# Kernel tuning notes

Hardware: AMD Instinct MI355X
Metric: run time of the kernel (lower is better)

## Reference

```python
import jax, jax.numpy as jnp
import numpy as np

TAU_PLUS = 0.02
TAU_MINUS = 0.02
TAU_X = 0.101
A_TRIPLET = 0.0065
HOMEOSTATIC_RATE = 0.1
DT = 0.001
SPIKE_P = 0.05  # spike probability used to binarize inputs


def setup_inputs() -> dict:
    key = jax.random.key(0)
    k1, k2, k3 = jax.random.split(key, 3)
    B, P, Q, T = 16, 2048, 2048, 256
    pre_spikes = (jax.random.uniform(k1, (B, P, T)) < SPIKE_P).astype(jnp.float32)
    post_spikes = (jax.random.uniform(k2, (B, Q, T)) < SPIKE_P).astype(jnp.float32)
    weights = jax.random.normal(k3, (P, Q), dtype=jnp.float32) * 0.1
    meta_A_plus = jnp.float32(0.01)
    meta_A_minus = jnp.float32(0.012)
    return {"pre_spikes": pre_spikes, "post_spikes": post_spikes,
            "weights": weights, "meta_A_plus": meta_A_plus,
            "meta_A_minus": meta_A_minus}


def _traces(spikes_tbn, decay):
    """Trace value used at step t: x_t = decay * (x_{t-1} + s_{t-1}), x_0 = 0."""
    def step(carry, s):
        x = decay * carry          # decayed trace, used for this step's update
        return x + s, x            # spike added AFTER the update, per original
    init = jnp.zeros(spikes_tbn.shape[1:], spikes_tbn.dtype)
    _, xs = jax.lax.scan(step, init, spikes_tbn)
    return xs  # [T, B, N]


def reference(pre_spikes, post_spikes, weights, meta_A_plus, meta_A_minus):
    B, P, T = pre_spikes.shape
    exp_plus = jnp.exp(jnp.float32(-DT / TAU_PLUS))
    exp_minus = jnp.exp(jnp.float32(-DT / TAU_MINUS))
    exp_x = jnp.exp(jnp.float32(-DT / TAU_X))

    pre_t = jnp.transpose(pre_spikes, (2, 0, 1))    # [T, B, P]
    post_t = jnp.transpose(post_spikes, (2, 0, 1))  # [T, B, Q]

    x_pre = _traces(pre_t, exp_plus)     # [T, B, P]
    x_post = _traces(post_t, exp_minus)  # [T, B, Q]
    x_trip = _traces(post_t, exp_x)      # [T, B, Q]

    # Per-step outer products summed over time == one big contraction over (t, b).
    ltp = jnp.einsum('tbp,tbq->pq', x_pre, post_t) * meta_A_plus
    triplet = jnp.einsum('tbp,tbq->pq', x_pre, post_t * x_trip) * A_TRIPLET
    ltd = jnp.einsum('tbp,tbq->pq', pre_t, x_post) * meta_A_minus
    weight_updates = ltp + triplet - ltd

    # Homeostatic scaling (fresh module: activity history holds only this sample)
    current_activity = (pre_spikes.sum() + post_spikes.sum()) / (B * T)
    scaling_factor = jnp.sqrt(HOMEOSTATIC_RATE / (current_activity + 1e-6))

    updated_weights = weights + weight_updates * scaling_factor
    return jnp.clip(updated_weights, -2.0, 2.0)
```

## Files before the change

kernel.cpp:

```cpp
#include <hip/hip_runtime.h>


constexpr int TB = 16;
constexpr int NP = 2048;
constexpr int NQ = 2048;
constexpr int TT = 256;
constexpr int KH = TB * TT;
constexpr int KT = 2 * KH;

typedef unsigned short ushort_t;
typedef __attribute__((ext_vector_type(8))) __bf16 bf16x8;
typedef __attribute__((ext_vector_type(4))) float f32x4;

__device__ __forceinline__ unsigned bf1(float f) {
    unsigned u = __builtin_bit_cast(unsigned, f);
    return (u + 0x7FFFu + ((u >> 16) & 1u)) >> 16;
}
__device__ __forceinline__ unsigned pack2(float lo, float hi) {
    return bf1(lo) | (bf1(hi) << 16);
}
__device__ __forceinline__ unsigned spk2(float a, float b) {
    return ((a != 0.f) ? 0x3F80u : 0u) | ((b != 0.f) ? 0x3F800000u : 0u);
}

constexpr float DF1 = 0.95122942450071400910f;
constexpr float DF2 = DF1 * DF1;
constexpr float DF4 = DF2 * DF2;
constexpr float DF8 = DF4 * DF4;
constexpr float DF16 = DF8 * DF8;
constexpr float DF32 = DF16 * DF16;
constexpr float DF64 = DF32 * DF32;

constexpr float DX1 = 0.99014786386058731819f;
constexpr float DX2 = DX1 * DX1;
constexpr float DX4 = DX2 * DX2;
constexpr float DX8 = DX4 * DX4;
constexpr float DX16 = DX8 * DX8;
constexpr float DX32 = DX16 * DX16;
constexpr float DX64 = DX32 * DX32;

template <int K>
__device__ __forceinline__ float seg_step(float b, float pw, int sl) {
    float t = __shfl_up(b, K, 64);
    return (sl >= K) ? fmaf(pw, t, b) : b;
}
__device__ __forceinline__ float scan16(float c, float p1, float p2, float p4,
                                        float p8, int sl) {
    c = seg_step<1>(c, p1, sl);
    c = seg_step<2>(c, p2, sl);
    c = seg_step<4>(c, p4, sl);
    c = seg_step<8>(c, p8, sl);
    return c;
}
__device__ __forceinline__ float fold4(float4 u, float d) {
    float C = d * u.x;
    C = d * (C + u.y); C = d * (C + u.z); C = d * (C + u.w);
    return C;
}
__device__ __forceinline__ float4 expand4(float x, float4 u, float d) {
    float4 t;
    t.x = x; x = d * (x + u.x);
    t.y = x; x = d * (x + u.y);
    t.z = x; x = d * (x + u.z);
    t.w = x;
    return t;
}

__global__ __launch_bounds__(256) void stage_traces(
    const float* __restrict__ pre, const float* __restrict__ post,
    const float* __restrict__ mApP, const float* __restrict__ mAmP,
    ushort_t* __restrict__ Ab, ushort_t* __restrict__ Bb,
    float* __restrict__ partials)
{
    const int tid  = threadIdx.x;
    const int lane = tid & 63;
    const int wv   = tid >> 6;
    const int sl   = lane & 15;
    const int rowg = blockIdx.x * 16 + wv * 4 + (lane >> 4);
    const bool isPre = rowg < TB * NP;
    const int m = isPre ? rowg : rowg - TB * NP;
    const int b = m >> 11;
    const int r = m & 2047;

    const float4* srcRow = (const float4*)((isPre ? pre : post) + (size_t)m * TT);
    const float4 u0 = srcRow[sl];
    const float4 u1 = srcRow[16 + sl];
    const float4 u2 = srcRow[32 + sl];
    const float4 u3 = srcRow[48 + sl];

    float cnt = ((u0.x + u0.y) + (u0.z + u0.w)) + ((u1.x + u1.y) + (u1.z + u1.w))
              + ((u2.x + u2.y) + (u2.z + u2.w)) + ((u3.x + u3.y) + (u3.z + u3.w));

    const int hi = lane | 15;

    float bf0 = scan16(fold4(u0, DF1), DF4, DF8, DF16, DF32, sl);
    float bf1_ = scan16(fold4(u1, DF1), DF4, DF8, DF16, DF32, sl);
    float bf2 = scan16(fold4(u2, DF1), DF4, DF8, DF16, DF32, sl);
    float bf3 = scan16(fold4(u3, DF1), DF4, DF8, DF16, DF32, sl);
    const float Tf0 = __shfl(bf0, hi, 64);
    const float Tf1 = __shfl(bf1_, hi, 64);
    const float Tf2 = __shfl(bf2, hi, 64);
    const float Xf1 = Tf0;
    const float Xf2 = fmaf(DF64, Xf1, Tf1);
    const float Xf3 = fmaf(DF64, Xf2, Tf2);
    float ef0 = __shfl_up(bf0, 1, 64);
    float ef1 = __shfl_up(bf1_, 1, 64);
    float ef2 = __shfl_up(bf2, 1, 64);
    float ef3 = __shfl_up(bf3, 1, 64);
    if (sl == 0) { ef0 = 0.f; ef1 = 0.f; ef2 = 0.f; ef3 = 0.f; }
    float pf = 1.f;
    if (sl & 1) pf *= DF4;
    if (sl & 2) pf *= DF8;
    if (sl & 4) pf *= DF16;
    if (sl & 8) pf *= DF32;
    const float4 t0 = expand4(ef0,                 u0, DF1);
    const float4 t1 = expand4(fmaf(pf, Xf1, ef1),  u1, DF1);
    const float4 t2 = expand4(fmaf(pf, Xf2, ef2),  u2, DF1);
    const float4 t3 = expand4(fmaf(pf, Xf3, ef3),  u3, DF1);

    ushort_t* oA = (isPre ? Ab : Bb) + (size_t)r * KT + b * TT + 4 * sl;

    if (isPre) {
        *(uint2*)(oA)            = uint2{pack2(t0.x, t0.y), pack2(t0.z, t0.w)};
        *(uint2*)(oA + 64)       = uint2{pack2(t1.x, t1.y), pack2(t1.z, t1.w)};
        *(uint2*)(oA + 128)      = uint2{pack2(t2.x, t2.y), pack2(t2.z, t2.w)};
        *(uint2*)(oA + 192)      = uint2{pack2(t3.x, t3.y), pack2(t3.z, t3.w)};
        *(uint2*)(oA + KH)       = uint2{spk2(u0.x, u0.y), spk2(u0.z, u0.w)};
        *(uint2*)(oA + KH + 64)  = uint2{spk2(u1.x, u1.y), spk2(u1.z, u1.w)};
        *(uint2*)(oA + KH + 128) = uint2{spk2(u2.x, u2.y), spk2(u2.z, u2.w)};
        *(uint2*)(oA + KH + 192) = uint2{spk2(u3.x, u3.y), spk2(u3.z, u3.w)};
    } else {
        float bx0 = scan16(fold4(u0, DX1), DX4, DX8, DX16, DX32, sl);
        float bx1 = scan16(fold4(u1, DX1), DX4, DX8, DX16, DX32, sl);
        float bx2 = scan16(fold4(u2, DX1), DX4, DX8, DX16, DX32, sl);
        float bx3 = scan16(fold4(u3, DX1), DX4, DX8, DX16, DX32, sl);
        const float Tx0 = __shfl(bx0, hi, 64);
        const float Tx1 = __shfl(bx1, hi, 64);
        const float Tx2 = __shfl(bx2, hi, 64);
        const float Xx1 = Tx0;
        const float Xx2 = fmaf(DX64, Xx1, Tx1);
        const float Xx3 = fmaf(DX64, Xx2, Tx2);
        float ex0 = __shfl_up(bx0, 1, 64);
        float ex1 = __shfl_up(bx1, 1, 64);
        float ex2 = __shfl_up(bx2, 1, 64);
        float ex3 = __shfl_up(bx3, 1, 64);
        if (sl == 0) { ex0 = 0.f; ex1 = 0.f; ex2 = 0.f; ex3 = 0.f; }
        float px = 1.f;
        if (sl & 1) px *= DX4;
        if (sl & 2) px *= DX8;
        if (sl & 4) px *= DX16;
        if (sl & 8) px *= DX32;
        const float4 w0 = expand4(ex0,                u0, DX1);
        const float4 w1 = expand4(fmaf(px, Xx1, ex1), u1, DX1);
        const float4 w2 = expand4(fmaf(px, Xx2, ex2), u2, DX1);
        const float4 w3 = expand4(fmaf(px, Xx3, ex3), u3, DX1);

        const float Ap = *mApP;
        const float Am = *mAmP;
        auto av2 = [&](float sa, float ta, float sb, float tb) -> unsigned {
            unsigned lo = (sa != 0.f) ? bf1(fmaf(0.0065f, ta, Ap)) : 0u;
            unsigned hi2 = (sb != 0.f) ? bf1(fmaf(0.0065f, tb, Ap)) : 0u;
            return lo | (hi2 << 16);
        };
        *(uint2*)(oA)       = uint2{av2(u0.x, w0.x, u0.y, w0.y), av2(u0.z, w0.z, u0.w, w0.w)};
        *(uint2*)(oA + 64)  = uint2{av2(u1.x, w1.x, u1.y, w1.y), av2(u1.z, w1.z, u1.w, w1.w)};
        *(uint2*)(oA + 128) = uint2{av2(u2.x, w2.x, u2.y, w2.y), av2(u2.z, w2.z, u2.w, w2.w)};
        *(uint2*)(oA + 192) = uint2{av2(u3.x, w3.x, u3.y, w3.y), av2(u3.z, w3.z, u3.w, w3.w)};
        *(uint2*)(oA + KH)       = uint2{pack2(-Am * t0.x, -Am * t0.y), pack2(-Am * t0.z, -Am * t0.w)};
        *(uint2*)(oA + KH + 64)  = uint2{pack2(-Am * t1.x, -Am * t1.y), pack2(-Am * t1.z, -Am * t1.w)};
        *(uint2*)(oA + KH + 128) = uint2{pack2(-Am * t2.x, -Am * t2.y), pack2(-Am * t2.z, -Am * t2.w)};
        *(uint2*)(oA + KH + 192) = uint2{pack2(-Am * t3.x, -Am * t3.y), pack2(-Am * t3.z, -Am * t3.w)};
    }

    #pragma unroll
    for (int off = 32; off > 0; off >>= 1)
        cnt += __shfl_down(cnt, off, 64);
    __shared__ float wsum[4];
    if (lane == 0) wsum[wv] = cnt;
    __syncthreads();
    if (tid == 0)
        partials[blockIdx.x] = (wsum[0] + wsum[1]) + (wsum[2] + wsum[3]);
}

__device__ __forceinline__ void async16(const ushort_t* g, ushort_t* l) {
    __builtin_amdgcn_global_load_lds(
        (const __attribute__((address_space(1))) unsigned int*)g,
        (__attribute__((address_space(3))) unsigned int*)l,
        16, 0, 0);
}

__global__ __launch_bounds__(256, 2) void gemm_split(
    const ushort_t* __restrict__ Ab, const ushort_t* __restrict__ Bb,
    const float* __restrict__ sp, float* __restrict__ scaleBuf,
    float* __restrict__ P0, float* __restrict__ P1)
{
    __shared__ ushort_t As[2][128 * 64];
    __shared__ ushort_t Bs[2][128 * 64];
    __shared__ float red[4];

    const int tid  = threadIdx.x;
    const int lane = tid & 63;
    const int wv   = tid >> 6;
    const int wr   = wv >> 1;
    const int wc   = wv & 1;
    const int quad = lane >> 4;
    const int m16  = lane & 15;

    if (blockIdx.x == 0) {
        float v = 0.f;
        #pragma unroll
        for (int i = 0; i < 16; ++i) v += sp[tid + i * 256];
        #pragma unroll
        for (int off = 32; off > 0; off >>= 1)
            v += __shfl_down(v, off, 64);
        if (lane == 0) red[wv] = v;
        __syncthreads();
        if (tid == 0) {
            float s = (red[0] + red[1]) + (red[2] + red[3]);
            scaleBuf[0] = sqrtf(0.1f / (s * (1.0f / 4096.0f) + 1e-6f));
        }
    }

    const int id  = blockIdx.x;
    const int xcd = id & 7;
    const int j5  = id >> 3;
    const int z   = j5 & 1;
    const int t   = j5 >> 1;
    const int pt  = ((xcd >> 1) << 2) + (t >> 3);
    const int qt  = ((xcd & 1) << 3) + (t & 7);

    const int p0 = pt * 128;
    const int q0 = qt * 128;
    const int kbase = z * (KT / 2);
    const int ldsbase = wv * 512;

    const ushort_t* gaP[4];
    const ushort_t* gbP[4];
    #pragma unroll
    for (int rr = 0; rr < 4; ++rr) {
        const int c   = rr * 256 + tid;
        const int row = c >> 3;
        const int kk8 = (c & 7) ^ (row & 7);
        gaP[rr] = Ab + (size_t)(p0 + row) * KT + kbase + kk8 * 8;
        gbP[rr] = Bb + (size_t)(q0 + row) * KT + kbase + kk8 * 8;
    }

    f32x4 acc[4][4] = {};

    auto stageF = [&](int buf) {
        #pragma unroll
        for (int rr = 0; rr < 4; ++rr) {
            async16(gaP[rr], &As[buf][rr * 2048 + ldsbase]);
            async16(gbP[rr], &Bs[buf][rr * 2048 + ldsbase]);
            gaP[rr] += 64;
            gbP[rr] += 64;
        }
    };
    auto computeF = [&](int buf) {
        #pragma unroll
        for (int ks = 0; ks < 2; ++ks) {
            bf16x8 af[4], bfr[4];
            #pragma unroll
            for (int i = 0; i < 4; ++i) {
                const int row  = wr * 64 + i * 16 + m16;
                const int slot = (ks * 4 + quad) ^ (row & 7);
                af[i] = *(const bf16x8*)&As[buf][row * 64 + slot * 8];
            }
            #pragma unroll
            for (int jj = 0; jj < 4; ++jj) {
                const int row  = wc * 64 + jj * 16 + m16;
                const int slot = (ks * 4 + quad) ^ (row & 7);
                bfr[jj] = *(const bf16x8*)&Bs[buf][row * 64 + slot * 8];
            }
            #pragma unroll
            for (int i = 0; i < 4; ++i)
                #pragma unroll
                for (int jj = 0; jj < 4; ++jj)
                    acc[i][jj] = __builtin_amdgcn_mfma_f32_16x16x32_bf16(
                        af[i], bfr[jj], acc[i][jj], 0, 0, 0);
        }
    };

    constexpr int NIT = (KT / 2) / 64;
    stageF(0);
    for (int kt2 = 0; kt2 < NIT / 2; ++kt2) {
        __syncthreads();
        stageF(1);
        computeF(0);
        __syncthreads();
        if (kt2 + 1 < NIT / 2)
            stageF(0);
        computeF(1);
    }

    float* P = z ? P1 : P0;
    #pragma unroll
    for (int i = 0; i < 4; ++i) {
        const int prow = p0 + wr * 64 + i * 16 + quad * 4;
        #pragma unroll
        for (int jj = 0; jj < 4; ++jj) {
            const int qcol = q0 + wc * 64 + jj * 16 + m16;
            #pragma unroll
            for (int r2 = 0; r2 < 4; ++r2)
                P[(size_t)(prow + r2) * NQ + qcol] = acc[i][jj][r2];
        }
    }
}

__global__ __launch_bounds__(256) void merge_out(
    const float* __restrict__ W, const float* __restrict__ P1,
    const float* __restrict__ scaleBuf, float* __restrict__ Out)
{
    const float scale = scaleBuf[0];
    const size_t i4 = (size_t)blockIdx.x * 256 + threadIdx.x;
    float4 w = ((const float4*)W)[i4];
    float4 a = ((const float4*)Out)[i4];
    float4 c = ((const float4*)P1)[i4];
    float4 o;
    o.x = fminf(fmaxf(fmaf(scale, a.x + c.x, w.x), -2.f), 2.f);
    o.y = fminf(fmaxf(fmaf(scale, a.y + c.y, w.y), -2.f), 2.f);
    o.z = fminf(fmaxf(fmaf(scale, a.z + c.z, w.z), -2.f), 2.f);
    o.w = fminf(fmaxf(fmaf(scale, a.w + c.w, w.w), -2.f), 2.f);
    ((float4*)Out)[i4] = o;
}

extern "C" void kernel_launch(void* const* d_in, const int* in_sizes, int n_in,
                              void* d_out, int out_size, void* d_ws, size_t ws_size,
                              hipStream_t stream) {
    const float* pre  = (const float*)d_in[0];
    const float* post = (const float*)d_in[1];
    const float* W    = (const float*)d_in[2];
    const float* mAp  = (const float*)d_in[3];
    const float* mAm  = (const float*)d_in[4];
    float* out = (float*)d_out;

    char* ws = (char*)d_ws;
    float* partials = (float*)ws;
    float* scaleBuf = (float*)(ws + 16384);
    ushort_t* Ab = (ushort_t*)(ws + 32768);
    ushort_t* Bb = (ushort_t*)(ws + 32768 + (size_t)NP * KT * 2);
    float* P1    = (float*)(ws + 32768 + 2 * (size_t)NP * KT * 2);

    stage_traces<<<dim3((TB * NP + TB * NQ) / 16), dim3(256), 0, stream>>>(
        pre, post, mAp, mAm, Ab, Bb, partials);

    gemm_split<<<dim3(512), dim3(256), 0, stream>>>(
        Ab, Bb, partials, scaleBuf, out, P1);

    merge_out<<<dim3(NP * NQ / 1024), dim3(256), 0, stream>>>(
        W, P1, scaleBuf, out);
}
```

Measured before the change: 200.2 us.

## Add 256x256-tile 8-wave GEMM with 4-way split-K and ping-pong schedule

Adds a new 512-thread GEMM that computes a 256x256 output tile per block, splits K four ways, and maps blocks to XCDs so neighbouring tiles share L2. Its main loop interleaves LDS reads, async global-to-LDS staging and MFMA quarter-blocks, separated by explicit barriers and waitcnts and raised with setprio. The larger tile raises operand reuse and cuts global traffic. The cost is an extra partial buffer pair to write and merge in a four-input merge kernel. The new path runs only when the workspace is large enough, otherwise the old 128x128 split-2 path is used.

```diff
diff --git a/kernel.cpp b/kernel.cpp
--- a/kernel.cpp
+++ b/kernel.cpp
@@ -189,13 +189,192 @@
         16, 0, 0);
 }
 
+#define FENCE() asm volatile("" ::: "memory")
+#define BAR()   do { FENCE(); __builtin_amdgcn_s_barrier(); FENCE(); } while (0)
+#define LGKM0() asm volatile("s_waitcnt lgkmcnt(0)" ::: "memory")
+#define VMC2()  asm volatile("s_waitcnt vmcnt(2)" ::: "memory")
+#define VMC0()  asm volatile("s_waitcnt vmcnt(0)" ::: "memory")
+
+#define STAGE(GP, LP, KI, H) do {                                           \
+    const ushort_t* _g = (GP) + (size_t)(H) * 128 * KT + (size_t)(KI) * 64; \
+    ushort_t* _l = (LP) + (H) * 8192;                                       \
+    async16(_g + ofG,  _l + ld0);                                           \
+    async16(_g + ofG2, _l + ld1);                                           \
+} while (0)
+
+#define RD_A(BUF, QM) do {                                                  \
+    _Pragma("unroll")                                                       \
+    for (int mi = 0; mi < 4; ++mi) {                                        \
+        const ushort_t* _r = &As[BUF][aBase + (QM) * 4096 + mi * 1024];     \
+        af[mi][0] = *(const bf16x8*)(_r + sK0);                             \
+        af[mi][1] = *(const bf16x8*)(_r + sK1);                             \
+    }                                                                       \
+} while (0)
+
+#define RD_B(BUF, QN, BV) do {                                              \
+    _Pragma("unroll")                                                       \
+    for (int ni = 0; ni < 2; ++ni) {                                        \
+        const ushort_t* _r = &Bs[BUF][bBase + (QN) * 2048 + ni * 1024];     \
+        BV[ni][0] = *(const bf16x8*)(_r + sK0);                             \
+        BV[ni][1] = *(const bf16x8*)(_r + sK1);                             \
+    }                                                                       \
+} while (0)
+
+#define MFMAQ(QM, QN, BV) do {                                              \
+    __builtin_amdgcn_s_setprio(1);                                          \
+    _Pragma("unroll")                                                       \
+    for (int ks = 0; ks < 2; ++ks)                                          \
+        _Pragma("unroll")                                                   \
+        for (int mi = 0; mi < 4; ++mi)                                      \
+            _Pragma("unroll")                                               \
+            for (int ni = 0; ni < 2; ++ni)                                  \
+                acc[(QM)*4+mi][(QN)*2+ni] =                                 \
+                    __builtin_amdgcn_mfma_f32_16x16x32_bf16(                \
+                        af[mi][ks], BV[ni][ks],                             \
+                        acc[(QM)*4+mi][(QN)*2+ni], 0, 0, 0);                \
+    __builtin_amdgcn_s_setprio(0);                                          \
+} while (0)
+
+__global__ __launch_bounds__(512) void gemm8(
+    const ushort_t* __restrict__ Ab, const ushort_t* __restrict__ Bb,
+    const float* __restrict__ sp, float* __restrict__ scaleBuf,
+    float* __restrict__ P0, float* __restrict__ P1,
+    float* __restrict__ P2, float* __restrict__ P3)
+{
+    __shared__ ushort_t As[2][256 * 64];
+    __shared__ ushort_t Bs[2][256 * 64];
+    __shared__ float red[8];
+
+    const int tid  = threadIdx.x;
+    const int lane = tid & 63;
+    const int wv   = tid >> 6;
+    const int wr   = wv >> 2;
+    const int wc   = wv & 3;
+    const int quad = lane >> 4;
+    const int m16  = lane & 15;
+
+    if (blockIdx.x == 0) {
+        float v = 0.f;
+        #pragma unroll
+        for (int i = 0; i < 8; ++i) v += sp[tid + i * 512];
+        #pragma unroll
+        for (int off = 32; off > 0; off >>= 1)
+            v += __shfl_down(v, off, 64);
+        if (lane == 0) red[wv] = v;
+        __syncthreads();
+        if (tid == 0) {
+            float s = ((red[0] + red[1]) + (red[2] + red[3]))
+                    + ((red[4] + red[5]) + (red[6] + red[7]));
+            scaleBuf[0] = sqrtf(0.1f / (s * (1.0f / 4096.0f) + 1e-6f));
+        }
+    }
+
+    const int id  = blockIdx.x;
+    const int xcd = id & 7;
+    const int j   = id >> 3;
+    const int z   = j & 3;
+    const int t   = j >> 2;
+    const int pt  = ((xcd >> 1) << 1) | (t >> 2);
+    const int qt  = ((xcd & 1) << 2) | (t & 3);
+    const int p0  = pt * 256;
+    const int q0  = qt * 256;
+    const int kbase = z * (KT / 4);
+
+    const ushort_t* Agp = Ab + (size_t)p0 * KT + kbase;
+    const ushort_t* Bgp = Bb + (size_t)q0 * KT + kbase;
+    const int rIn  = tid >> 3;
+    const int rIn2 = rIn + 64;
+    const size_t ofG  = (size_t)rIn  * KT + (size_t)((((tid & 7) ^ (rIn  & 7))) * 8);
+    const size_t ofG2 = (size_t)rIn2 * KT + (size_t)((((tid & 7) ^ (rIn2 & 7))) * 8);
+    const int ld0 = tid * 8;
+    const int ld1 = 4096 + tid * 8;
+
+    const int x8  = (m16 & 7) * 8;
+    const int sK0 = (quad * 8) ^ x8;
+    const int sK1 = ((quad + 4) * 8) ^ x8;
+    const int aBase = (wr * 128 + m16) * 64;
+    const int bBase = (wc * 64 + m16) * 64;
+
+    f32x4 acc[8][4] = {};
+    bf16x8 af[4][2], bv0[2][2], bv1[2][2];
+
+    STAGE(Agp, As[0], 0, 0);
+    STAGE(Agp, As[0], 0, 1);
+    STAGE(Bgp, Bs[0], 0, 0);
+    STAGE(Bgp, Bs[0], 0, 1);
+    STAGE(Agp, As[1], 1, 0);
+    VMC2();
+    BAR();
+
+    #pragma unroll 1
+    for (int it = 0; it < 16; ++it) {
+        const int k2 = 2 * it;
+        RD_A(0, 0);
+        RD_B(0, 0, bv0);
+        STAGE(Agp, As[1], k2 + 1, 1);
+        STAGE(Bgp, Bs[1], k2 + 1, 0);
+        BAR(); LGKM0();
+        MFMAQ(0, 0, bv0);
+        BAR();
+        RD_B(0, 1, bv1);
+        STAGE(Bgp, Bs[1], k2 + 1, 1);
+        BAR(); LGKM0();
+        MFMAQ(0, 1, bv1);
+        BAR();
+        RD_A(0, 1);
+        BAR(); LGKM0();
+        MFMAQ(1, 1, bv1);
+        BAR();
+        RD_B(0, 0, bv0);
+        if (it < 15) STAGE(Agp, As[0], k2 + 2, 0);
+        BAR(); LGKM0();
+        MFMAQ(1, 0, bv0);
+        if (it < 15) { VMC2(); } else { VMC0(); }
+        BAR();
+        RD_A(1, 0);
+        RD_B(1, 0, bv0);
+        if (it < 15) { STAGE(Agp, As[0], k2 + 2, 1); STAGE(Bgp, Bs[0], k2 + 2, 0); }
+        BAR(); LGKM0();
+        MFMAQ(0, 0, bv0);
+        BAR();
+        RD_B(1, 1, bv1);
+        if (it < 15) STAGE(Bgp, Bs[0], k2 + 2, 1);
+        BAR(); LGKM0();
+        MFMAQ(0, 1, bv1);
+        BAR();
+        RD_A(1, 1);
+        BAR(); LGKM0();
+        MFMAQ(1, 1, bv1);
+        BAR();
+        RD_B(1, 0, bv0);
+        if (it < 15) STAGE(Agp, As[1], k2 + 3, 0);
+        BAR(); LGKM0();
+        MFMAQ(1, 0, bv0);
+        if (it < 15) { VMC2(); }
+        BAR();
+    }
+
+    float* P = (z == 0) ? P0 : ((z == 1) ? P1 : ((z == 2) ? P2 : P3));
+    #pragma unroll
+    for (int m = 0; m < 8; ++m) {
+        const int prow = p0 + wr * 128 + m * 16 + quad * 4;
+        #pragma unroll
+        for (int n = 0; n < 4; ++n) {
+            const int qcol = q0 + wc * 64 + n * 16 + m16;
+            #pragma unroll
+            for (int r = 0; r < 4; ++r)
+                P[(size_t)(prow + r) * NQ + qcol] = acc[m][n][r];
+        }
+    }
+}
+
 __global__ __launch_bounds__(256, 2) void gemm_split(
     const ushort_t* __restrict__ Ab, const ushort_t* __restrict__ Bb,
     const float* __restrict__ sp, float* __restrict__ scaleBuf,
     float* __restrict__ P0, float* __restrict__ P1)
 {
-    __shared__ ushort_t As[2][128 * 64];
-    __shared__ ushort_t Bs[2][128 * 64];
+    __shared__ ushort_t Ls[2][128 * 64];
+    __shared__ ushort_t Rs[2][128 * 64];
     __shared__ float red[4];
 
     const int tid  = threadIdx.x;
@@ -250,8 +429,8 @@
     auto stageF = [&](int buf) {
         #pragma unroll
         for (int rr = 0; rr < 4; ++rr) {
-            async16(gaP[rr], &As[buf][rr * 2048 + ldsbase]);
-            async16(gbP[rr], &Bs[buf][rr * 2048 + ldsbase]);
+            async16(gaP[rr], &Ls[buf][rr * 2048 + ldsbase]);
+            async16(gbP[rr], &Rs[buf][rr * 2048 + ldsbase]);
             gaP[rr] += 64;
             gbP[rr] += 64;
         }
@@ -259,25 +438,25 @@
     auto computeF = [&](int buf) {
         #pragma unroll
         for (int ks = 0; ks < 2; ++ks) {
-            bf16x8 af[4], bfr[4];
+            bf16x8 afl[4], bfr[4];
             #pragma unroll
             for (int i = 0; i < 4; ++i) {
                 const int row  = wr * 64 + i * 16 + m16;
                 const int slot = (ks * 4 + quad) ^ (row & 7);
-                af[i] = *(const bf16x8*)&As[buf][row * 64 + slot * 8];
+                afl[i] = *(const bf16x8*)&Ls[buf][row * 64 + slot * 8];
             }
             #pragma unroll
             for (int jj = 0; jj < 4; ++jj) {
                 const int row  = wc * 64 + jj * 16 + m16;
                 const int slot = (ks * 4 + quad) ^ (row & 7);
-                bfr[jj] = *(const bf16x8*)&Bs[buf][row * 64 + slot * 8];
+                bfr[jj] = *(const bf16x8*)&Rs[buf][row * 64 + slot * 8];
             }
             #pragma unroll
             for (int i = 0; i < 4; ++i)
                 #pragma unroll
                 for (int jj = 0; jj < 4; ++jj)
                     acc[i][jj] = __builtin_amdgcn_mfma_f32_16x16x32_bf16(
-                        af[i], bfr[jj], acc[i][jj], 0, 0, 0);
+                        afl[i], bfr[jj], acc[i][jj], 0, 0, 0);
         }
     };
 
@@ -307,7 +486,27 @@
     }
 }
 
-__global__ __launch_bounds__(256) void merge_out(
+__global__ __launch_bounds__(256) void merge_out4(
+    const float* __restrict__ W, const float* __restrict__ P1,
+    const float* __restrict__ P2, const float* __restrict__ P3,
+    const float* __restrict__ scaleBuf, float* __restrict__ Out)
+{
+    const float scale = scaleBuf[0];
+    const size_t i4 = (size_t)blockIdx.x * 256 + threadIdx.x;
+    float4 w = ((const float4*)W)[i4];
+    float4 a = ((const float4*)Out)[i4];
+    float4 b = ((const float4*)P1)[i4];
+    float4 c = ((const float4*)P2)[i4];
+    float4 d = ((const float4*)P3)[i4];
+    float4 o;
+    o.x = fminf(fmaxf(fmaf(scale, (a.x + b.x) + (c.x + d.x), w.x), -2.f), 2.f);
+    o.y = fminf(fmaxf(fmaf(scale, (a.y + b.y) + (c.y + d.y), w.y), -2.f), 2.f);
+    o.z = fminf(fmaxf(fmaf(scale, (a.z + b.z) + (c.z + d.z), w.z), -2.f), 2.f);
+    o.w = fminf(fmaxf(fmaf(scale, (a.w + b.w) + (c.w + d.w), w.w), -2.f), 2.f);
+    ((float4*)Out)[i4] = o;
+}
+
+__global__ __launch_bounds__(256) void merge_out2(
     const float* __restrict__ W, const float* __restrict__ P1,
     const float* __restrict__ scaleBuf, float* __restrict__ Out)
 {
@@ -334,19 +533,30 @@
     const float* mAm  = (const float*)d_in[4];
     float* out = (float*)d_out;
 
+    const size_t AB = (size_t)NP * KT * 2;
+    const size_t PB = (size_t)NP * NQ * 4;
+
     char* ws = (char*)d_ws;
     float* partials = (float*)ws;
     float* scaleBuf = (float*)(ws + 16384);
     ushort_t* Ab = (ushort_t*)(ws + 32768);
-    ushort_t* Bb = (ushort_t*)(ws + 32768 + (size_t)NP * KT * 2);
-    float* P1    = (float*)(ws + 32768 + 2 * (size_t)NP * KT * 2);
+    ushort_t* Bb = (ushort_t*)(ws + 32768 + AB);
+    float* P1 = (float*)(ws + 32768 + 2 * AB);
+    float* P2 = (float*)(ws + 32768 + 2 * AB + PB);
+    float* P3 = (float*)(ws + 32768 + 2 * AB + 2 * PB);
 
     stage_traces<<<dim3((TB * NP + TB * NQ) / 16), dim3(256), 0, stream>>>(
         pre, post, mAp, mAm, Ab, Bb, partials);
 
-    gemm_split<<<dim3(512), dim3(256), 0, stream>>>(
-        Ab, Bb, partials, scaleBuf, out, P1);
-
-    merge_out<<<dim3(NP * NQ / 1024), dim3(256), 0, stream>>>(
-        W, P1, scaleBuf, out);
-}
+    if (ws_size >= 32768 + 2 * AB + 3 * PB) {
+        gemm8<<<dim3(256), dim3(512), 0, stream>>>(
+            Ab, Bb, partials, scaleBuf, out, P1, P2, P3);
+        merge_out4<<<dim3(NP * NQ / 1024), dim3(256), 0, stream>>>(
+            W, P1, P2, P3, scaleBuf, out);
+    } else {
+        gemm_split<<<dim3(512), dim3(256), 0, stream>>>(
+            Ab, Bb, partials, scaleBuf, out, P1);
+        merge_out2<<<dim3(NP * NQ / 1024), dim3(256), 0, stream>>>(
+            W, P1, scaleBuf, out);
+    }
+}
```

After: 209.7 us. +4.8%, slower.

## Fuse split-K reduction and epilogue into GEMM via per-tile atomic counter

Applied to the files above, without the earlier changes.

Each split-K tile pair now writes its partial product and bumps a per-tile atomic counter. The second block to finish reads the other partial, computes the homeostatic scale itself, and writes the clipped final output, so the separate merge kernel and one full pass over the output are no longer needed. The counters are zeroed by the staging kernel. This trades an extra partial buffer, threadfence and atomic overhead, and a serial tail in the last-arriving block, for one fewer launch and less global traffic. It falls back to the old path when the workspace is too small.

```diff
diff --git a/kernel.cpp b/kernel.cpp
--- a/kernel.cpp
+++ b/kernel.cpp
@@ -70,9 +70,11 @@
     const float* __restrict__ pre, const float* __restrict__ post,
     const float* __restrict__ mApP, const float* __restrict__ mAmP,
     ushort_t* __restrict__ Ab, ushort_t* __restrict__ Bb,
-    float* __restrict__ partials)
+    float* __restrict__ partials, int* __restrict__ cnt)
 {
     const int tid  = threadIdx.x;
+    if (blockIdx.x == 0) cnt[tid] = 0;
+
     const int lane = tid & 63;
     const int wv   = tid >> 6;
     const int sl   = lane & 15;
@@ -88,8 +90,8 @@
     const float4 u2 = srcRow[32 + sl];
     const float4 u3 = srcRow[48 + sl];
 
-    float cnt = ((u0.x + u0.y) + (u0.z + u0.w)) + ((u1.x + u1.y) + (u1.z + u1.w))
-              + ((u2.x + u2.y) + (u2.z + u2.w)) + ((u3.x + u3.y) + (u3.z + u3.w));
+    float cnt_s = ((u0.x + u0.y) + (u0.z + u0.w)) + ((u1.x + u1.y) + (u1.z + u1.w))
+                + ((u2.x + u2.y) + (u2.z + u2.w)) + ((u3.x + u3.y) + (u3.z + u3.w));
 
     const int hi = lane | 15;
 
@@ -174,9 +176,9 @@
 
     #pragma unroll
     for (int off = 32; off > 0; off >>= 1)
-        cnt += __shfl_down(cnt, off, 64);
+        cnt_s += __shfl_down(cnt_s, off, 64);
     __shared__ float wsum[4];
-    if (lane == 0) wsum[wv] = cnt;
+    if (lane == 0) wsum[wv] = cnt_s;
     __syncthreads();
     if (tid == 0)
         partials[blockIdx.x] = (wsum[0] + wsum[1]) + (wsum[2] + wsum[3]);
@@ -189,14 +191,16 @@
         16, 0, 0);
 }
 
-__global__ __launch_bounds__(256, 2) void gemm_split(
+__global__ __launch_bounds__(256, 2) void gemm_fz(
     const ushort_t* __restrict__ Ab, const ushort_t* __restrict__ Bb,
-    const float* __restrict__ sp, float* __restrict__ scaleBuf,
-    float* __restrict__ P0, float* __restrict__ P1)
+    const float* __restrict__ sp, const float* __restrict__ W,
+    float* __restrict__ P0, float* __restrict__ P1,
+    int* __restrict__ cnt, float* __restrict__ Out)
 {
-    __shared__ ushort_t As[2][128 * 64];
-    __shared__ ushort_t Bs[2][128 * 64];
+    __shared__ ushort_t Ls[2][128 * 64];
+    __shared__ ushort_t Rs[2][128 * 64];
     __shared__ float red[4];
+    __shared__ int tk;
 
     const int tid  = threadIdx.x;
     const int lane = tid & 63;
@@ -206,21 +210,6 @@
     const int quad = lane >> 4;
     const int m16  = lane & 15;
 
-    if (blockIdx.x == 0) {
-        float v = 0.f;
-        #pragma unroll
-        for (int i = 0; i < 16; ++i) v += sp[tid + i * 256];
-        #pragma unroll
-        for (int off = 32; off > 0; off >>= 1)
-            v += __shfl_down(v, off, 64);
-        if (lane == 0) red[wv] = v;
-        __syncthreads();
-        if (tid == 0) {
-            float s = (red[0] + red[1]) + (red[2] + red[3]);
-            scaleBuf[0] = sqrtf(0.1f / (s * (1.0f / 4096.0f) + 1e-6f));
-        }
-    }
-
     const int id  = blockIdx.x;
     const int xcd = id & 7;
     const int j5  = id >> 3;
@@ -250,8 +239,8 @@
     auto stageF = [&](int buf) {
         #pragma unroll
         for (int rr = 0; rr < 4; ++rr) {
-            async16(gaP[rr], &As[buf][rr * 2048 + ldsbase]);
-            async16(gbP[rr], &Bs[buf][rr * 2048 + ldsbase]);
+            async16(gaP[rr], &Ls[buf][rr * 2048 + ldsbase]);
+            async16(gbP[rr], &Rs[buf][rr * 2048 + ldsbase]);
             gaP[rr] += 64;
             gbP[rr] += 64;
         }
@@ -259,25 +248,25 @@
     auto computeF = [&](int buf) {
         #pragma unroll
         for (int ks = 0; ks < 2; ++ks) {
-            bf16x8 af[4], bfr[4];
+            bf16x8 afl[4], bfr[4];
             #pragma unroll
             for (int i = 0; i < 4; ++i) {
                 const int row  = wr * 64 + i * 16 + m16;
                 const int slot = (ks * 4 + quad) ^ (row & 7);
-                af[i] = *(const bf16x8*)&As[buf][row * 64 + slot * 8];
+                afl[i] = *(const bf16x8*)&Ls[buf][row * 64 + slot * 8];
             }
             #pragma unroll
             for (int jj = 0; jj < 4; ++jj) {
                 const int row  = wc * 64 + jj * 16 + m16;
                 const int slot = (ks * 4 + quad) ^ (row & 7);
-                bfr[jj] = *(const bf16x8*)&Bs[buf][row * 64 + slot * 8];
+                bfr[jj] = *(const bf16x8*)&Rs[buf][row * 64 + slot * 8];
             }
             #pragma unroll
             for (int i = 0; i < 4; ++i)
                 #pragma unroll
                 for (int jj = 0; jj < 4; ++jj)
                     acc[i][jj] = __builtin_amdgcn_mfma_f32_16x16x32_bf16(
-                        af[i], bfr[jj], acc[i][jj], 0, 0, 0);
+                        afl[i], bfr[jj], acc[i][jj], 0, 0, 0);
         }
     };
 
@@ -305,9 +294,159 @@
                 P[(size_t)(prow + r2) * NQ + qcol] = acc[i][jj][r2];
         }
     }
-}
-
-__global__ __launch_bounds__(256) void merge_out(
+    __threadfence();
+    if (tid == 0) tk = atomicAdd(&cnt[pt * 16 + qt], 1);
+    __syncthreads();
+    if (tk == 0) return;
+    __threadfence();
+
+    float v = 0.f;
+    #pragma unroll
+    for (int i = 0; i < 16; ++i) v += sp[tid + i * 256];
+    #pragma unroll
+    for (int off = 32; off > 0; off >>= 1)
+        v += __shfl_down(v, off, 64);
+    if (lane == 0) red[wv] = v;
+    __syncthreads();
+    const float s = (red[0] + red[1]) + (red[2] + red[3]);
+    const float scale = sqrtf(0.1f / (s * (1.0f / 4096.0f) + 1e-6f));
+
+    const float* Ps = z ? P0 : P1;
+    #pragma unroll
+    for (int i = 0; i < 4; ++i) {
+        const int prow = p0 + wr * 64 + i * 16 + quad * 4;
+        #pragma unroll
+        for (int jj = 0; jj < 4; ++jj) {
+            const int qcol = q0 + wc * 64 + jj * 16 + m16;
+            #pragma unroll
+            for (int r2 = 0; r2 < 4; ++r2) {
+                const size_t idx = (size_t)(prow + r2) * NQ + qcol;
+                const float sum = acc[i][jj][r2] + Ps[idx];
+                Out[idx] = fminf(fmaxf(fmaf(scale, sum, W[idx]), -2.f), 2.f);
+            }
+        }
+    }
+}
+
+__global__ __launch_bounds__(256, 2) void gemm_split(
+    const ushort_t* __restrict__ Ab, const ushort_t* __restrict__ Bb,
+    const float* __restrict__ sp, float* __restrict__ scaleBuf,
+    float* __restrict__ P0, float* __restrict__ P1)
+{
+    __shared__ ushort_t Ls[2][128 * 64];
+    __shared__ ushort_t Rs[2][128 * 64];
+    __shared__ float red[4];
+
+    const int tid  = threadIdx.x;
+    const int lane = tid & 63;
+    const int wv   = tid >> 6;
+    const int wr   = wv >> 1;
+    const int wc   = wv & 1;
+    const int quad = lane >> 4;
+    const int m16  = lane & 15;
+
+    if (blockIdx.x == 0) {
+        float v = 0.f;
+        #pragma unroll
+        for (int i = 0; i < 16; ++i) v += sp[tid + i * 256];
+        #pragma unroll
+        for (int off = 32; off > 0; off >>= 1)
+            v += __shfl_down(v, off, 64);
+        if (lane == 0) red[wv] = v;
+        __syncthreads();
+        if (tid == 0) {
+            float s = (red[0] + red[1]) + (red[2] + red[3]);
+            scaleBuf[0] = sqrtf(0.1f / (s * (1.0f / 4096.0f) + 1e-6f));
+        }
+    }
+
+    const int id  = blockIdx.x;
+    const int xcd = id & 7;
+    const int j5  = id >> 3;
+    const int z   = j5 & 1;
+    const int t   = j5 >> 1;
+    const int pt  = ((xcd >> 1) << 2) + (t >> 3);
+    const int qt  = ((xcd & 1) << 3) + (t & 7);
+
+    const int p0 = pt * 128;
+    const int q0 = qt * 128;
+    const int kbase = z * (KT / 2);
+    const int ldsbase = wv * 512;
+
+    const ushort_t* gaP[4];
+    const ushort_t* gbP[4];
+    #pragma unroll
+    for (int rr = 0; rr < 4; ++rr) {
+        const int c   = rr * 256 + tid;
+        const int row = c >> 3;
+        const int kk8 = (c & 7) ^ (row & 7);
+        gaP[rr] = Ab + (size_t)(p0 + row) * KT + kbase + kk8 * 8;
+        gbP[rr] = Bb + (size_t)(q0 + row) * KT + kbase + kk8 * 8;
+    }
+
+    f32x4 acc[4][4] = {};
+
+    auto stageF = [&](int buf) {
+        #pragma unroll
+        for (int rr = 0; rr < 4; ++rr) {
+            async16(gaP[rr], &Ls[buf][rr * 2048 + ldsbase]);
+            async16(gbP[rr], &Rs[buf][rr * 2048 + ldsbase]);
+            gaP[rr] += 64;
+            gbP[rr] += 64;
+        }
+    };
+    auto computeF = [&](int buf) {
+        #pragma unroll
+        for (int ks = 0; ks < 2; ++ks) {
+            bf16x8 afl[4], bfr[4];
+            #pragma unroll
+            for (int i = 0; i < 4; ++i) {
+                const int row  = wr * 64 + i * 16 + m16;
+                const int slot = (ks * 4 + quad) ^ (row & 7);
+                afl[i] = *(const bf16x8*)&Ls[buf][row * 64 + slot * 8];
+            }
+            #pragma unroll
+            for (int jj = 0; jj < 4; ++jj) {
+                const int row  = wc * 64 + jj * 16 + m16;
+                const int slot = (ks * 4 + quad) ^ (row & 7);
+                bfr[jj] = *(const bf16x8*)&Rs[buf][row * 64 + slot * 8];
+            }
+            #pragma unroll
+            for (int i = 0; i < 4; ++i)
+                #pragma unroll
+                for (int jj = 0; jj < 4; ++jj)
+                    acc[i][jj] = __builtin_amdgcn_mfma_f32_16x16x32_bf16(
+                        afl[i], bfr[jj], acc[i][jj], 0, 0, 0);
+        }
+    };
+
+    constexpr int NIT = (KT / 2) / 64;
+    stageF(0);
+    for (int kt2 = 0; kt2 < NIT / 2; ++kt2) {
+        __syncthreads();
+        stageF(1);
+        computeF(0);
+        __syncthreads();
+        if (kt2 + 1 < NIT / 2)
+            stageF(0);
+        computeF(1);
+    }
+
+    float* P = z ? P1 : P0;
+    #pragma unroll
+    for (int i = 0; i < 4; ++i) {
+        const int prow = p0 + wr * 64 + i * 16 + quad * 4;
+        #pragma unroll
+        for (int jj = 0; jj < 4; ++jj) {
+            const int qcol = q0 + wc * 64 + jj * 16 + m16;
+            #pragma unroll
+            for (int r2 = 0; r2 < 4; ++r2)
+                P[(size_t)(prow + r2) * NQ + qcol] = acc[i][jj][r2];
+        }
+    }
+}
+
+__global__ __launch_bounds__(256) void merge_out2(
     const float* __restrict__ W, const float* __restrict__ P1,
     const float* __restrict__ scaleBuf, float* __restrict__ Out)
 {
@@ -334,19 +473,28 @@
     const float* mAm  = (const float*)d_in[4];
     float* out = (float*)d_out;
 
+    const size_t AB = (size_t)NP * KT * 2;
+    const size_t PB = (size_t)NP * NQ * 4;
+
     char* ws = (char*)d_ws;
     float* partials = (float*)ws;
     float* scaleBuf = (float*)(ws + 16384);
+    int*   cnt      = (int*)(ws + 20480);
     ushort_t* Ab = (ushort_t*)(ws + 32768);
-    ushort_t* Bb = (ushort_t*)(ws + 32768 + (size_t)NP * KT * 2);
-    float* P1    = (float*)(ws + 32768 + 2 * (size_t)NP * KT * 2);
+    ushort_t* Bb = (ushort_t*)(ws + 32768 + AB);
+    float* Pa = (float*)(ws + 32768 + 2 * AB);
+    float* Pb = (float*)(ws + 32768 + 2 * AB + PB);
 
     stage_traces<<<dim3((TB * NP + TB * NQ) / 16), dim3(256), 0, stream>>>(
-        pre, post, mAp, mAm, Ab, Bb, partials);
-
-    gemm_split<<<dim3(512), dim3(256), 0, stream>>>(
-        Ab, Bb, partials, scaleBuf, out, P1);
-
-    merge_out<<<dim3(NP * NQ / 1024), dim3(256), 0, stream>>>(
-        W, P1, scaleBuf, out);
-}
+        pre, post, mAp, mAm, Ab, Bb, partials, cnt);
+
+    if (ws_size >= 32768 + 2 * AB + 2 * PB) {
+        gemm_fz<<<dim3(512), dim3(256), 0, stream>>>(
+            Ab, Bb, partials, W, Pa, Pb, cnt, out);
+    } else {
+        gemm_split<<<dim3(512), dim3(256), 0, stream>>>(
+            Ab, Bb, partials, scaleBuf, out, Pa);
+        merge_out2<<<dim3(NP * NQ / 1024), dim3(256), 0, stream>>>(
+            W, Pa, scaleBuf, out);
+    }
+}
```

Result: slower. 321.2 us (+60.4%).

## Replace split-K GEMM with full-K 128x64 tiles and fused epilogue

Applied to the files above, without the earlier changes.

Drops the two-way split-K partial GEMM and its separate merge kernel. Each block now computes a 128x64 output tile over the full K range, then reduces the spike-count partials itself to get the homeostatic scale and writes clip(W + scale*acc) directly. This removes the fp32 partial write/read traffic and one kernel launch. In exchange each block runs twice as many K iterations on a narrower tile with lower MFMA density per LDS load, and every block redundantly sums the scale partials.

```diff
diff --git a/kernel.cpp b/kernel.cpp
--- a/kernel.cpp
+++ b/kernel.cpp
@@ -189,13 +189,13 @@
         16, 0, 0);
 }
 
-__global__ __launch_bounds__(256, 2) void gemm_split(
+__global__ __launch_bounds__(256, 2) void gemm_nk(
     const ushort_t* __restrict__ Ab, const ushort_t* __restrict__ Bb,
-    const float* __restrict__ sp, float* __restrict__ scaleBuf,
-    float* __restrict__ P0, float* __restrict__ P1)
+    const float* __restrict__ sp, const float* __restrict__ W,
+    float* __restrict__ Out)
 {
     __shared__ ushort_t As[2][128 * 64];
-    __shared__ ushort_t Bs[2][128 * 64];
+    __shared__ ushort_t Bs[2][64 * 64];
     __shared__ float red[4];
 
     const int tid  = threadIdx.x;
@@ -206,60 +206,51 @@
     const int quad = lane >> 4;
     const int m16  = lane & 15;
 
-    if (blockIdx.x == 0) {
-        float v = 0.f;
-        #pragma unroll
-        for (int i = 0; i < 16; ++i) v += sp[tid + i * 256];
-        #pragma unroll
-        for (int off = 32; off > 0; off >>= 1)
-            v += __shfl_down(v, off, 64);
-        if (lane == 0) red[wv] = v;
-        __syncthreads();
-        if (tid == 0) {
-            float s = (red[0] + red[1]) + (red[2] + red[3]);
-            scaleBuf[0] = sqrtf(0.1f / (s * (1.0f / 4096.0f) + 1e-6f));
-        }
-    }
-
     const int id  = blockIdx.x;
     const int xcd = id & 7;
-    const int j5  = id >> 3;
-    const int z   = j5 & 1;
-    const int t   = j5 >> 1;
-    const int pt  = ((xcd >> 1) << 2) + (t >> 3);
-    const int qt  = ((xcd & 1) << 3) + (t & 7);
+    const int t   = id >> 3;
+    const int pt  = ((xcd >> 1) << 2) | (t >> 4);
+    const int qt  = ((xcd & 1) << 4) | (t & 15);
 
     const int p0 = pt * 128;
-    const int q0 = qt * 128;
-    const int kbase = z * (KT / 2);
+    const int q0 = qt * 64;
     const int ldsbase = wv * 512;
 
     const ushort_t* gaP[4];
-    const ushort_t* gbP[4];
+    const ushort_t* gbP[2];
     #pragma unroll
     for (int rr = 0; rr < 4; ++rr) {
         const int c   = rr * 256 + tid;
         const int row = c >> 3;
         const int kk8 = (c & 7) ^ (row & 7);
-        gaP[rr] = Ab + (size_t)(p0 + row) * KT + kbase + kk8 * 8;
-        gbP[rr] = Bb + (size_t)(q0 + row) * KT + kbase + kk8 * 8;
-    }
-
-    f32x4 acc[4][4] = {};
+        gaP[rr] = Ab + (size_t)(p0 + row) * KT + kk8 * 8;
+    }
+    #pragma unroll
+    for (int rr = 0; rr < 2; ++rr) {
+        const int c   = rr * 256 + tid;
+        const int row = c >> 3;
+        const int kk8 = (c & 7) ^ (row & 7);
+        gbP[rr] = Bb + (size_t)(q0 + row) * KT + kk8 * 8;
+    }
+
+    f32x4 acc[4][2] = {};
 
     auto stageF = [&](int buf) {
         #pragma unroll
         for (int rr = 0; rr < 4; ++rr) {
             async16(gaP[rr], &As[buf][rr * 2048 + ldsbase]);
+            gaP[rr] += 64;
+        }
+        #pragma unroll
+        for (int rr = 0; rr < 2; ++rr) {
             async16(gbP[rr], &Bs[buf][rr * 2048 + ldsbase]);
-            gaP[rr] += 64;
             gbP[rr] += 64;
         }
     };
     auto computeF = [&](int buf) {
         #pragma unroll
         for (int ks = 0; ks < 2; ++ks) {
-            bf16x8 af[4], bfr[4];
+            bf16x8 af[4], bfr[2];
             #pragma unroll
             for (int i = 0; i < 4; ++i) {
                 const int row  = wr * 64 + i * 16 + m16;
@@ -267,21 +258,21 @@
                 af[i] = *(const bf16x8*)&As[buf][row * 64 + slot * 8];
             }
             #pragma unroll
-            for (int jj = 0; jj < 4; ++jj) {
-                const int row  = wc * 64 + jj * 16 + m16;
+            for (int jj = 0; jj < 2; ++jj) {
+                const int row  = wc * 32 + jj * 16 + m16;
                 const int slot = (ks * 4 + quad) ^ (row & 7);
                 bfr[jj] = *(const bf16x8*)&Bs[buf][row * 64 + slot * 8];
             }
             #pragma unroll
             for (int i = 0; i < 4; ++i)
                 #pragma unroll
-                for (int jj = 0; jj < 4; ++jj)
+                for (int jj = 0; jj < 2; ++jj)
                     acc[i][jj] = __builtin_amdgcn_mfma_f32_16x16x32_bf16(
                         af[i], bfr[jj], acc[i][jj], 0, 0, 0);
         }
     };
 
-    constexpr int NIT = (KT / 2) / 64;
+    constexpr int NIT = KT / 64;
     stageF(0);
     for (int kt2 = 0; kt2 < NIT / 2; ++kt2) {
         __syncthreads();
@@ -293,35 +284,31 @@
         computeF(1);
     }
 
-    float* P = z ? P1 : P0;
+    float v = 0.f;
+    #pragma unroll
+    for (int i = 0; i < 16; ++i) v += sp[tid + i * 256];
+    #pragma unroll
+    for (int off = 32; off > 0; off >>= 1)
+        v += __shfl_down(v, off, 64);
+    if (lane == 0) red[wv] = v;
+    __syncthreads();
+    const float s = (red[0] + red[1]) + (red[2] + red[3]);
+    const float scale = sqrtf(0.1f / (s * (1.0f / 4096.0f) + 1e-6f));
+
     #pragma unroll
     for (int i = 0; i < 4; ++i) {
         const int prow = p0 + wr * 64 + i * 16 + quad * 4;
         #pragma unroll
-        for (int jj = 0; jj < 4; ++jj) {
-            const int qcol = q0 + wc * 64 + jj * 16 + m16;
+        for (int jj = 0; jj < 2; ++jj) {
+            const int qcol = q0 + wc * 32 + jj * 16 + m16;
             #pragma unroll
-            for (int r2 = 0; r2 < 4; ++r2)
-                P[(size_t)(prow + r2) * NQ + qcol] = acc[i][jj][r2];
+            for (int r2 = 0; r2 < 4; ++r2) {
+                const size_t idx = (size_t)(prow + r2) * NQ + qcol;
+                Out[idx] = fminf(fmaxf(fmaf(scale, acc[i][jj][r2], W[idx]),
+                                       -2.f), 2.f);
+            }
         }
     }
-}
-
-__global__ __launch_bounds__(256) void merge_out(
-    const float* __restrict__ W, const float* __restrict__ P1,
-    const float* __restrict__ scaleBuf, float* __restrict__ Out)
-{
-    const float scale = scaleBuf[0];
-    const size_t i4 = (size_t)blockIdx.x * 256 + threadIdx.x;
-    float4 w = ((const float4*)W)[i4];
-    float4 a = ((const float4*)Out)[i4];
-    float4 c = ((const float4*)P1)[i4];
-    float4 o;
-    o.x = fminf(fmaxf(fmaf(scale, a.x + c.x, w.x), -2.f), 2.f);
-    o.y = fminf(fmaxf(fmaf(scale, a.y + c.y, w.y), -2.f), 2.f);
-    o.z = fminf(fmaxf(fmaf(scale, a.z + c.z, w.z), -2.f), 2.f);
-    o.w = fminf(fmaxf(fmaf(scale, a.w + c.w, w.w), -2.f), 2.f);
-    ((float4*)Out)[i4] = o;
 }
 
 extern "C" void kernel_launch(void* const* d_in, const int* in_sizes, int n_in,
@@ -336,17 +323,12 @@
 
     char* ws = (char*)d_ws;
     float* partials = (float*)ws;
-    float* scaleBuf = (float*)(ws + 16384);
     ushort_t* Ab = (ushort_t*)(ws + 32768);
     ushort_t* Bb = (ushort_t*)(ws + 32768 + (size_t)NP * KT * 2);
-    float* P1    = (float*)(ws + 32768 + 2 * (size_t)NP * KT * 2);
 
     stage_traces<<<dim3((TB * NP + TB * NQ) / 16), dim3(256), 0, stream>>>(
         pre, post, mAp, mAm, Ab, Bb, partials);
 
-    gemm_split<<<dim3(512), dim3(256), 0, stream>>>(
-        Ab, Bb, partials, scaleBuf, out, P1);
-
-    merge_out<<<dim3(NP * NQ / 1024), dim3(256), 0, stream>>>(
-        W, P1, scaleBuf, out);
-}
+    gemm_nk<<<dim3(512), dim3(256), 0, stream>>>(
+        Ab, Bb, partials, W, out);
+}
```

After: 223.3 us. 11.6% more time.
